# Optimization experiments

Hardware: AMD Instinct MI355X
Metric: run time of the kernel (lower is better)

The kernel has to match this reference:

```python
import jax, jax.numpy as jnp
import numpy as np
from jax import lax

NEG_INF = -1e18
T, K, U = 8192, 24, 104


def setup_inputs() -> dict:
    key = jax.random.key(0)
    k1, k2, k3, k4, k5 = jax.random.split(key, 5)
    emission_logprobs = jax.random.normal(k1, (T, K), dtype=jnp.float32)
    quality_weights = jax.random.uniform(k2, (T,), dtype=jnp.float32)
    log_pi = jax.nn.log_softmax(jax.random.normal(k3, (K,), dtype=jnp.float32))
    log_A = jax.nn.log_softmax(jax.random.normal(k4, (K, K), dtype=jnp.float32), axis=1)
    log_D = jax.nn.log_softmax(jax.random.normal(k5, (K, U), dtype=jnp.float32), axis=1)
    # explicit-duration HSMM: self-transitions disallowed (durations model dwell time)
    transition_mask = 1 - jnp.eye(K, dtype=jnp.int32)
    return {"emission_logprobs": emission_logprobs, "quality_weights": quality_weights,
            "log_pi": log_pi, "log_A": log_A, "log_D": log_D,
            "transition_mask": transition_mask}


def _segment_scores(emission, qw):
    # seg[t, u_idx, s] = sum_{k=t-u+1..t} qw[k]*B[k,s], u = u_idx+1; NEG_INF if u > t+1
    weighted = emission * qw[:, None]
    cum = jnp.concatenate([jnp.zeros((1, K), emission.dtype), jnp.cumsum(weighted, 0)], 0)  # [T+1,K]
    t_idx = jnp.arange(T)
    u = jnp.arange(1, U + 1)
    start = t_idx[:, None] + 1 - u[None, :]              # [T,U]
    valid = start >= 0
    seg = cum[t_idx + 1][:, None, :] - cum[jnp.clip(start, 0)]  # [T,U,K]
    return jnp.where(valid[:, :, None], seg, NEG_INF)


def _forward_backward(emission, qw, log_pi, log_A_m, log_D):
    seg = _segment_scores(emission, qw)  # [T,U,K]
    log_D_T = log_D.T                    # [U,K]
    u_idx = jnp.arange(U)

    # ---- forward DP over t (carry = last U alpha rows) ----
    alpha0 = log_pi + log_D[:, 0] + emission[0]
    buf0 = jnp.full((U, K), NEG_INF, emission.dtype).at[-1].set(alpha0)

    def fstep(buf, t):
        prev = buf[::-1]  # prev[u_idx] = alpha[t-1-u_idx] (NEG_INF for times < 0)
        trans = jax.nn.logsumexp(prev[:, :, None] + log_A_m[None, :, :], axis=1)  # [U,K]
        # entry_time = t-1-u_idx < 0  <=>  u_idx >= t : use initial-state score
        inner = jnp.where((u_idx >= t)[:, None], log_pi[None, :], trans)
        alpha_t = jax.nn.logsumexp(inner + log_D_T + seg[t], axis=0)  # [K]
        return jnp.concatenate([buf[1:], alpha_t[None]], 0), alpha_t

    _, alphas = lax.scan(fstep, buf0, jnp.arange(1, T))
    alpha = jnp.concatenate([alpha0[None], alphas], 0)

    # ---- backward DP (carry buf[i] = beta[t+1+i]) ----
    bbuf0 = jnp.full((U, K), NEG_INF, emission.dtype).at[0].set(0.0)

    def bstep(buf, t):
        ends = t + 1 + u_idx
        valid = ends <= T - 1
        segv = seg[jnp.clip(ends, 0, T - 1), u_idx, :]                 # [U,K]
        inner = jnp.where(valid[:, None], log_D_T + segv + buf, NEG_INF)
        m = jax.nn.logsumexp(inner, axis=0)                            # [K] over durations
        beta_t = jax.nn.logsumexp(log_A_m + m[None, :], axis=1)        # [K] over next state
        return jnp.concatenate([beta_t[None], buf[:-1]], 0), beta_t

    _, betas = lax.scan(bstep, bbuf0, jnp.arange(T - 2, -1, -1))
    beta = jnp.concatenate([betas[::-1], jnp.zeros((1, K), emission.dtype)], 0)
    return alpha, beta


def reference(emission_logprobs, quality_weights, log_pi, log_A, log_D, transition_mask):
    log_A_m = jnp.where(transition_mask.astype(bool), log_A, NEG_INF)
    alpha, beta = _forward_backward(emission_logprobs, quality_weights, log_pi, log_A_m, log_D)
    # posterior_decode: gamma = alpha + beta, normalized over states
    return jax.nn.softmax(alpha + beta, axis=1)
```

## Files before the change

### kernel.cpp

```cpp
#include <hip/hip_runtime.h>
#include <math.h>

#define TT 8192
#define KK 24
#define UU 104
#define NEGINF (-1e18f)
#define INV_LN2 1.4426950408889634f

__device__ __forceinline__ float exp2_(float x) {
#if __has_builtin(__builtin_amdgcn_exp2f)
  return __builtin_amdgcn_exp2f(x);
#else
  return exp2f(x);
#endif
}

template<int CTRL>
__device__ __forceinline__ float dppf(float x) {
  return __builtin_bit_cast(float,
    __builtin_amdgcn_update_dpp(0, __builtin_bit_cast(int, x), CTRL, 0xF, 0xF, true));
}
__device__ __forceinline__ float red16_sum(float v) {
  v += dppf<0xB1>(v);
  v += dppf<0x4E>(v);
  v += dppf<0x124>(v);
  v += dppf<0x128>(v);
  return v;
}
__device__ __forceinline__ float ror1(float x) { return dppf<0x121>(x); }

__global__ __launch_bounds__(256) void cumsum_kernel(
    const float* __restrict__ em, const float* __restrict__ qw,
    float* __restrict__ cum)
{
  const int k = blockIdx.x;
  const int tid = threadIdx.x;
  const int lane = tid & 63;
  const int wid = tid >> 6;
  __shared__ float wsum[4];
  float carry = 0.0f;
  if (tid == 0) cum[k] = 0.0f;
  for (int c = 0; c < TT / 256; ++c) {
    int t = c * 256 + tid;
    float v = em[t * KK + k] * (qw[t] * INV_LN2);
    #pragma unroll
    for (int d = 1; d < 64; d <<= 1) {
      float tmp = __shfl_up(v, d);
      if (lane >= d) v += tmp;
    }
    if (lane == 63) wsum[wid] = v;
    __syncthreads();
    float off = carry;
    #pragma unroll
    for (int w = 0; w < 4; ++w)
      if (w < wid) off += wsum[w];
    cum[(size_t)(t + 1) * KK + k] = off + v;
    carry += wsum[0] + wsum[1] + wsum[2] + wsum[3];
    __syncthreads();
  }
}

__global__ __launch_bounds__(384, 1) void scan_kernel(
    const float* __restrict__ em,
    const float* __restrict__ log_pi,
    const float* __restrict__ log_A,
    const float* __restrict__ log_D,
    const float* __restrict__ cum,
    float* __restrict__ alpha_out,
    float* __restrict__ beta_out)
{
  __shared__ __align__(16) float xbuf[2][32];
  const int tid = threadIdx.x;
  const int g = tid >> 4;
  const int L = tid & 15;
  const bool l0 = (L == 0);
  const int j1 = 2 * L, j2 = 2 * L + 1;

  if (tid < 8) { xbuf[0][24 + tid] = 0.0f; xbuf[1][24 + tid] = 0.0f; }

  float ld0 = log_D[g * UU + L] * INV_LN2;
  float ld1 = log_D[g * UU + L + 16] * INV_LN2;
  float ld2 = log_D[g * UU + L + 32] * INV_LN2;
  float ld3 = log_D[g * UU + L + 48] * INV_LN2;
  float ld4 = log_D[g * UU + L + 64] * INV_LN2;
  float ld5 = log_D[g * UU + L + 80] * INV_LN2;
  float ld6 = (L < 8) ? log_D[g * UU + L + 96] * INV_LN2 : NEGINF;

  if (blockIdx.x == 0) {
    float Ak1 = (j1 < KK && j1 != g) ? log_A[j1 * KK + g] * INV_LN2 : NEGINF;
    float Ak2 = (j2 < KK && j2 != g) ? log_A[j2 * KK + g] * INV_LN2 : NEGINF;
    float lpi2 = log_pi[g] * INV_LN2;
    float a0 = lpi2 + log_D[g * UU] * INV_LN2 + em[g] * INV_LN2;
    if (l0) { alpha_out[g] = a0; xbuf[0][g] = a0; }
    float P0 = l0 ? lpi2 : NEGINF;
    float P1 = NEGINF, P2 = NEGINF, P3 = NEGINF,
          P4 = NEGINF, P5 = NEGINF, P6 = NEGINF;
    float ccur = cum[1 * KK + g], c1 = cum[2 * KK + g],
          c2 = cum[3 * KK + g],  c3 = cum[4 * KK + g];
    float Mh = a0;
    float Ua = a0 - ccur;
    __syncthreads();
    for (int t = 1; t < TT; ++t) {
      int tp = t + 4; if (tp > TT) tp = TT;
      float c4 = cum[(size_t)tp * KK + g];
      float r0 = ror1(P0), r1 = ror1(P1), r2 = ror1(P2), r3 = ror1(P3),
            r4 = ror1(P4), r5 = ror1(P5), r6 = ror1(P6);
      P1 = l0 ? r0 : r1;  P2 = l0 ? r1 : r2;  P3 = l0 ? r2 : r3;
      P4 = l0 ? r3 : r4;  P5 = l0 ? r4 : r5;  P6 = l0 ? r5 : r6;
      float e1 = exp2_(P1 + (ld1 - Ua));
      float e2 = exp2_(P2 + (ld2 - Ua));
      float e3 = exp2_(P3 + (ld3 - Ua));
      float e4 = exp2_(P4 + (ld4 - Ua));
      float e5 = exp2_(P5 + (ld5 - Ua));
      float e6 = exp2_(P6 + (ld6 - Ua));
      float e0nz = exp2_(r0 + (ld0 - Ua));
      float srest = ((e1 + e2) + (e3 + e4)) + (e5 + e6);
      float2 av = *(const float2*)&xbuf[(t - 1) & 1][j1];
      float w1 = av.x + (Ak1 - Mh);
      float w2 = av.y + (Ak2 - Mh);
      float s1 = red16_sum(exp2_(w1) + exp2_(w2));
      float gamma = Mh + __log2f(s1);
      Mh = gamma;
      float phi = gamma - ccur;
      P0 = l0 ? phi : r0;
      float e0 = l0 ? exp2_(phi + (ld0 - Ua)) : e0nz;
      float S = red16_sum(e0 + srest);
      float ua = Ua + __log2f(S);
      float a = c1 + ua;
      Ua = ua;
      if (l0) { xbuf[t & 1][g] = a; alpha_out[(size_t)t * KK + g] = a; }
      ccur = c1; c1 = c2; c2 = c3; c3 = c4;
      __syncthreads();
    }
  } else {
    float Bj1 = (j1 < KK && j1 != g) ? log_A[g * KK + j1] * INV_LN2 : NEGINF;
    float Bj2 = (j2 < KK && j2 != g) ? log_A[g * KK + j2] * INV_LN2 : NEGINF;
    float cT = cum[(size_t)TT * KK + g];
    if (l0) beta_out[(size_t)(TT - 1) * KK + g] = 0.0f;
    float Q0 = l0 ? cT : NEGINF;
    float Q1 = NEGINF, Q2 = NEGINF, Q3 = NEGINF,
          Q4 = NEGINF, Q5 = NEGINF, Q6 = NEGINF;
    float c1 = cum[(size_t)(TT - 1) * KK + g];
    float d1 = cum[(size_t)(TT - 2) * KK + g];
    float d2 = cum[(size_t)(TT - 3) * KK + g];
    float nh = cT;
    float bh = 0.0f;
    __syncthreads();
    for (int t = TT - 2; t >= 0; --t) {
      int tp = t - 2; if (tp < 0) tp = 0;
      float d3 = cum[(size_t)tp * KK + g];
      float x0 = exp2_(Q0 + (ld0 - nh));
      float x1 = exp2_(Q1 + (ld1 - nh));
      float x2 = exp2_(Q2 + (ld2 - nh));
      float x3 = exp2_(Q3 + (ld3 - nh));
      float x4 = exp2_(Q4 + (ld4 - nh));
      float x5 = exp2_(Q5 + (ld5 - nh));
      float x6 = exp2_(Q6 + (ld6 - nh));
      float sA = red16_sum(((x0 + x1) + (x2 + x3)) + ((x4 + x5) + x6));
      float n = nh + __log2f(sA);
      nh = n;
      float m = n - c1;
      if (l0) xbuf[t & 1][g] = m;
      __syncthreads();
      float2 mv = *(const float2*)&xbuf[t & 1][j1];
      float y1 = mv.x + (Bj1 - bh);
      float y2 = mv.y + (Bj2 - bh);
      float sB = red16_sum(exp2_(y1) + exp2_(y2));
      float bt = bh + __log2f(sB);
      bh = bt;
      float psi = c1 + bt;
      if (l0) beta_out[(size_t)t * KK + g] = bt;
      float q0 = ror1(Q0), q1 = ror1(Q1), q2 = ror1(Q2), q3 = ror1(Q3),
            q4 = ror1(Q4), q5 = ror1(Q5), q6 = ror1(Q6);
      Q6 = l0 ? q5 : q6;  Q5 = l0 ? q4 : q5;  Q4 = l0 ? q3 : q4;
      Q3 = l0 ? q2 : q3;  Q2 = l0 ? q1 : q2;  Q1 = l0 ? q0 : q1;
      Q0 = l0 ? psi : q0;
      c1 = d1; d1 = d2; d2 = d3;
    }
  }
}

__global__ __launch_bounds__(256) void softmax_kernel(
    float* __restrict__ ab, const float* __restrict__ beta)
{
  int t = blockIdx.x * 256 + threadIdx.x;
  float s[KK];
  float mx = -INFINITY;
  #pragma unroll
  for (int k = 0; k < KK; ++k) {
    s[k] = ab[(size_t)t * KK + k] + beta[(size_t)t * KK + k];
    mx = fmaxf(mx, s[k]);
  }
  float sum = 0.0f;
  #pragma unroll
  for (int k = 0; k < KK; ++k) { s[k] = exp2_(s[k] - mx); sum += s[k]; }
  float inv = 1.0f / sum;
  #pragma unroll
  for (int k = 0; k < KK; ++k) ab[(size_t)t * KK + k] = s[k] * inv;
}

extern "C" void kernel_launch(void* const* d_in, const int* in_sizes, int n_in,
                              void* d_out, int out_size, void* d_ws, size_t ws_size,
                              hipStream_t stream) {
  const float* em  = (const float*)d_in[0];
  const float* qw  = (const float*)d_in[1];
  const float* lpi = (const float*)d_in[2];
  const float* lA  = (const float*)d_in[3];
  const float* lD  = (const float*)d_in[4];

  float* out  = (float*)d_out;
  float* cum  = (float*)d_ws;
  float* beta = (float*)d_ws + (size_t)(TT + 1) * KK;

  cumsum_kernel<<<KK, 256, 0, stream>>>(em, qw, cum);
  scan_kernel<<<2, 384, 0, stream>>>(em, lpi, lA, lD, cum, out, beta);
  softmax_kernel<<<TT / 256, 256, 0, stream>>>(out, beta);
}
```

Before: 3.740 ms.

## Restructure HSMM scans to exchange linear-domain sums and shorten serial chain

Both forward and backward recurrences are reformulated so that the value exchanged through shared memory each step is a linear-domain normalized sum rather than a log value. Each lane tracks the per-state running log offsets of its neighbour states itself, so the exp/log work that used to sit between barriers is moved off the critical path. The per-step dependent chain becomes FMA plus DPP reduction plus a shared store and barrier, with the exps for the next step computed after the barrier. In exchange it adds clamping (CLMP, 1e-37 floors) and extra log2 calls per step, which carries some numerical risk under large dynamic range.

Result: slower. 4.765 ms (+27.4%).

```diff
diff --git a/kernel.cpp b/kernel.cpp
--- a/kernel.cpp
+++ b/kernel.cpp
@@ -6,6 +6,7 @@
 #define UU 104
 #define NEGINF (-1e18f)
 #define INV_LN2 1.4426950408889634f
+#define CLMP 60.0f
 
 __device__ __forceinline__ float exp2_(float x) {
 #if __has_builtin(__builtin_amdgcn_exp2f)
@@ -28,6 +29,14 @@
   return v;
 }
 __device__ __forceinline__ float ror1(float x) { return dppf<0x121>(x); }
+
+__device__ __forceinline__ float a0_of(const float* lp, const float* lD,
+                                       const float* em, int s) {
+  return (lp[s] * INV_LN2 + lD[s * UU] * INV_LN2) + em[s] * INV_LN2;
+}
+__device__ __forceinline__ float nh0_of(const float* lD, const float* cum, int s) {
+  return lD[s * UU] * INV_LN2 + cum[(size_t)TT * KK + s];
+}
 
 __global__ __launch_bounds__(256) void cumsum_kernel(
     const float* __restrict__ em, const float* __restrict__ qw,
@@ -75,8 +84,10 @@
   const int L = tid & 15;
   const bool l0 = (L == 0);
   const int j1 = 2 * L, j2 = 2 * L + 1;
-
-  if (tid < 8) { xbuf[0][24 + tid] = 0.0f; xbuf[1][24 + tid] = 0.0f; }
+  const bool vj = (j1 < KK);
+  const int jc = vj ? j1 : 0;
+
+  if (tid < 8) { xbuf[0][24 + tid] = 1.0f; xbuf[1][24 + tid] = 1.0f; }
 
   float ld0 = log_D[g * UU + L] * INV_LN2;
   float ld1 = log_D[g * UU + L + 16] * INV_LN2;
@@ -85,97 +96,169 @@
   float ld4 = log_D[g * UU + L + 64] * INV_LN2;
   float ld5 = log_D[g * UU + L + 80] * INV_LN2;
   float ld6 = (L < 8) ? log_D[g * UU + L + 96] * INV_LN2 : NEGINF;
+  float d0 = log_D[g * UU] * INV_LN2;
 
   if (blockIdx.x == 0) {
-    float Ak1 = (j1 < KK && j1 != g) ? log_A[j1 * KK + g] * INV_LN2 : NEGINF;
-    float Ak2 = (j2 < KK && j2 != g) ? log_A[j2 * KK + g] * INV_LN2 : NEGINF;
+    float Ak1 = (vj && j1 != g) ? log_A[j1 * KK + g] * INV_LN2 : NEGINF;
+    float Ak2 = (vj && j2 != g) ? log_A[j2 * KK + g] * INV_LN2 : NEGINF;
     float lpi2 = log_pi[g] * INV_LN2;
-    float a0 = lpi2 + log_D[g * UU] * INV_LN2 + em[g] * INV_LN2;
-    if (l0) { alpha_out[g] = a0; xbuf[0][g] = a0; }
+    float a0 = a0_of(log_pi, log_D, em, g);
+    float cc0 = cum[1 * KK + g], cc1 = cum[2 * KK + g],
+          cc2 = cum[3 * KK + g], cc3 = cum[4 * KK + g];
+    float2 pj1r = *(const float2*)&cum[1 * KK + jc];
+    float2 pjA = *(const float2*)&cum[2 * KK + jc];
+    float2 pjB = *(const float2*)&cum[3 * KK + jc];
+    float2 pjC = *(const float2*)&cum[4 * KK + jc];
+    float Ua = a0 - cc0;
+    float Uaj1 = vj ? (a0_of(log_pi, log_D, em, j1) - pj1r.x) : 0.f;
+    float Uaj2 = vj ? (a0_of(log_pi, log_D, em, j2) - pj1r.y) : 0.f;
+    float Mh = a0;
+    float f1 = exp2_(fminf((pj1r.x + Uaj1) + (Ak1 - Mh), CLMP));
+    float f2 = exp2_(fminf((pj1r.y + Uaj2) + (Ak2 - Mh), CLMP));
+    float fc = exp2_(fminf((Mh + d0) - (cc0 + Ua), CLMP));
+    float fc0 = l0 ? fc : 0.f;
     float P0 = l0 ? lpi2 : NEGINF;
     float P1 = NEGINF, P2 = NEGINF, P3 = NEGINF,
           P4 = NEGINF, P5 = NEGINF, P6 = NEGINF;
-    float ccur = cum[1 * KK + g], c1 = cum[2 * KK + g],
-          c2 = cum[3 * KK + g],  c3 = cum[4 * KK + g];
-    float Mh = a0;
-    float Ua = a0 - ccur;
-    __syncthreads();
-    for (int t = 1; t < TT; ++t) {
-      int tp = t + 4; if (tp > TT) tp = TT;
-      float c4 = cum[(size_t)tp * KK + g];
+    {
       float r0 = ror1(P0), r1 = ror1(P1), r2 = ror1(P2), r3 = ror1(P3),
             r4 = ror1(P4), r5 = ror1(P5), r6 = ror1(P6);
+      P0 = r0;
       P1 = l0 ? r0 : r1;  P2 = l0 ? r1 : r2;  P3 = l0 ? r2 : r3;
       P4 = l0 ? r3 : r4;  P5 = l0 ? r4 : r5;  P6 = l0 ? r5 : r6;
-      float e1 = exp2_(P1 + (ld1 - Ua));
-      float e2 = exp2_(P2 + (ld2 - Ua));
-      float e3 = exp2_(P3 + (ld3 - Ua));
-      float e4 = exp2_(P4 + (ld4 - Ua));
-      float e5 = exp2_(P5 + (ld5 - Ua));
-      float e6 = exp2_(P6 + (ld6 - Ua));
-      float e0nz = exp2_(r0 + (ld0 - Ua));
-      float srest = ((e1 + e2) + (e3 + e4)) + (e5 + e6);
-      float2 av = *(const float2*)&xbuf[(t - 1) & 1][j1];
-      float w1 = av.x + (Ak1 - Mh);
-      float w2 = av.y + (Ak2 - Mh);
-      float s1 = red16_sum(exp2_(w1) + exp2_(w2));
-      float gamma = Mh + __log2f(s1);
-      Mh = gamma;
-      float phi = gamma - ccur;
-      P0 = l0 ? phi : r0;
-      float e0 = l0 ? exp2_(phi + (ld0 - Ua)) : e0nz;
-      float S = red16_sum(e0 + srest);
-      float ua = Ua + __log2f(S);
-      float a = c1 + ua;
-      Ua = ua;
-      if (l0) { xbuf[t & 1][g] = a; alpha_out[(size_t)t * KK + g] = a; }
-      ccur = c1; c1 = c2; c2 = c3; c3 = c4;
+    }
+    float mU = 0.f - Ua;
+    float e0 = exp2_(P0 + (ld0 + mU));
+    float e1 = exp2_(P1 + (ld1 + mU));
+    float e2 = exp2_(P2 + (ld2 + mU));
+    float e3 = exp2_(P3 + (ld3 + mU));
+    float e4 = exp2_(P4 + (ld4 + mU));
+    float e5 = exp2_(P5 + (ld5 + mU));
+    float e6 = exp2_(P6 + (ld6 + mU));
+    float sloc = (((l0 ? 0.f : e0) + e1) + (e2 + e3)) + ((e4 + e5) + e6);
+    if (l0) alpha_out[g] = a0;
+    float2 Sjr; Sjr.x = 1.0f; Sjr.y = 1.0f;
+    __syncthreads();
+    #pragma unroll 1
+    for (int t = 1; t < TT; ++t) {
+      float w  = fmaf(Sjr.x, f1, Sjr.y * f2);
+      float sG = red16_sum(w);
+      float vv = fmaf(sG, fc0, sloc);
+      float S  = red16_sum(vv);
+      float Sp = fmaxf(S, 1e-37f);
+      if (l0) xbuf[t & 1][g] = Sp;
       __syncthreads();
+      float2 Sjn = *(const float2*)&xbuf[t & 1][j1];
+      int tp = (t + 4 <= TT) ? (t + 4) : TT;
+      float ccN = cum[(size_t)tp * KK + g];
+      float2 pjN = *(const float2*)&cum[(size_t)tp * KK + jc];
+      float lgG = __log2f(fmaxf(sG, 1e-37f));
+      float lgS = __log2f(Sp);
+      Mh += lgG;
+      float phi = Mh - cc0;
+      if (l0) alpha_out[(size_t)t * KK + g] = (cc1 + Ua) + lgS;
+      Ua += lgS;
+      Uaj1 += __log2f(Sjr.x);
+      Uaj2 += __log2f(Sjr.y);
+      f1 = exp2_(fminf((pjA.x + Uaj1) + (Ak1 - Mh), CLMP));
+      f2 = exp2_(fminf((pjA.y + Uaj2) + (Ak2 - Mh), CLMP));
+      fc = exp2_(fminf((Mh + d0) - (cc1 + Ua), CLMP));
+      fc0 = l0 ? fc : 0.f;
+      float P0i = l0 ? phi : P0;
+      float r0 = ror1(P0i), r1 = ror1(P1), r2 = ror1(P2), r3 = ror1(P3),
+            r4 = ror1(P4), r5 = ror1(P5), r6 = ror1(P6);
+      P0 = r0;
+      P1 = l0 ? r0 : r1;  P2 = l0 ? r1 : r2;  P3 = l0 ? r2 : r3;
+      P4 = l0 ? r3 : r4;  P5 = l0 ? r4 : r5;  P6 = l0 ? r5 : r6;
+      float mU2 = 0.f - Ua;
+      e0 = exp2_(P0 + (ld0 + mU2));
+      e1 = exp2_(P1 + (ld1 + mU2));
+      e2 = exp2_(P2 + (ld2 + mU2));
+      e3 = exp2_(P3 + (ld3 + mU2));
+      e4 = exp2_(P4 + (ld4 + mU2));
+      e5 = exp2_(P5 + (ld5 + mU2));
+      e6 = exp2_(P6 + (ld6 + mU2));
+      sloc = (((l0 ? 0.f : e0) + e1) + (e2 + e3)) + ((e4 + e5) + e6);
+      Sjr = Sjn;
+      cc0 = cc1; cc1 = cc2; cc2 = cc3; cc3 = ccN;
+      pjA = pjB; pjB = pjC; pjC = pjN;
     }
   } else {
-    float Bj1 = (j1 < KK && j1 != g) ? log_A[g * KK + j1] * INV_LN2 : NEGINF;
-    float Bj2 = (j2 < KK && j2 != g) ? log_A[g * KK + j2] * INV_LN2 : NEGINF;
+    float Cj1 = (vj && j1 != g) ? log_A[g * KK + j1] * INV_LN2 : NEGINF;
+    float Cj2 = (vj && j2 != g) ? log_A[g * KK + j2] * INV_LN2 : NEGINF;
     float cT = cum[(size_t)TT * KK + g];
-    if (l0) beta_out[(size_t)(TT - 1) * KK + g] = 0.0f;
+    float cA = cum[(size_t)(TT - 1) * KK + g];
+    float cB = cum[(size_t)(TT - 2) * KK + g];
+    float cC = cum[(size_t)(TT - 3) * KK + g];
+    float2 pj1b = *(const float2*)&cum[(size_t)(TT - 1) * KK + jc];
+    float2 pjB = *(const float2*)&cum[(size_t)(TT - 2) * KK + jc];
+    float2 pjC = *(const float2*)&cum[(size_t)(TT - 3) * KK + jc];
+    float Nh = nh0_of(log_D, cum, g);
+    float Nhj1 = vj ? nh0_of(log_D, cum, j1) : 0.f;
+    float Nhj2 = vj ? nh0_of(log_D, cum, j2) : 0.f;
+    float bh = 0.0f;
+    float f1 = exp2_(fminf((Nhj1 - pj1b.x) + Cj1, CLMP));
+    float f2 = exp2_(fminf((Nhj2 - pj1b.y) + Cj2, CLMP));
     float Q0 = l0 ? cT : NEGINF;
     float Q1 = NEGINF, Q2 = NEGINF, Q3 = NEGINF,
           Q4 = NEGINF, Q5 = NEGINF, Q6 = NEGINF;
-    float c1 = cum[(size_t)(TT - 1) * KK + g];
-    float d1 = cum[(size_t)(TT - 2) * KK + g];
-    float d2 = cum[(size_t)(TT - 3) * KK + g];
-    float nh = cT;
-    float bh = 0.0f;
+    float mN = 0.f - Nh;
+    float e0 = exp2_(Q0 + (ld0 + mN));
+    float e1 = exp2_(Q1 + (ld1 + mN));
+    float e2 = exp2_(Q2 + (ld2 + mN));
+    float e3 = exp2_(Q3 + (ld3 + mN));
+    float e4 = exp2_(Q4 + (ld4 + mN));
+    float e5 = exp2_(Q5 + (ld5 + mN));
+    float e6 = exp2_(Q6 + (ld6 + mN));
+    float slocB = ((e0 + e1) + (e2 + e3)) + ((e4 + e5) + e6);
+    float fb = 0.f, fb0 = 0.f, sBprev = 0.f;
+    float psi_prev = cT;
+    if (l0) beta_out[(size_t)(TT - 1) * KK + g] = 0.0f;
     __syncthreads();
+    #pragma unroll 1
     for (int t = TT - 2; t >= 0; --t) {
-      int tp = t - 2; if (tp < 0) tp = 0;
-      float d3 = cum[(size_t)tp * KK + g];
-      float x0 = exp2_(Q0 + (ld0 - nh));
-      float x1 = exp2_(Q1 + (ld1 - nh));
-      float x2 = exp2_(Q2 + (ld2 - nh));
-      float x3 = exp2_(Q3 + (ld3 - nh));
-      float x4 = exp2_(Q4 + (ld4 - nh));
-      float x5 = exp2_(Q5 + (ld5 - nh));
-      float x6 = exp2_(Q6 + (ld6 - nh));
-      float sA = red16_sum(((x0 + x1) + (x2 + x3)) + ((x4 + x5) + x6));
-      float n = nh + __log2f(sA);
-      nh = n;
-      float m = n - c1;
-      if (l0) xbuf[t & 1][g] = m;
+      float vA = fmaf(sBprev, fb0, slocB);
+      float SA = red16_sum(vA);
+      float SAp = fmaxf(SA, 1e-37f);
+      if (l0) xbuf[t & 1][g] = SAp;
       __syncthreads();
-      float2 mv = *(const float2*)&xbuf[t & 1][j1];
-      float y1 = mv.x + (Bj1 - bh);
-      float y2 = mv.y + (Bj2 - bh);
-      float sB = red16_sum(exp2_(y1) + exp2_(y2));
-      float bt = bh + __log2f(sB);
+      float2 SAj = *(const float2*)&xbuf[t & 1][j1];
+      int tm = (t - 2 >= 0) ? (t - 2) : 0;
+      float cN = cum[(size_t)tm * KK + g];
+      float2 pjN = *(const float2*)&cum[(size_t)tm * KK + jc];
+      float wb = fmaf(SAj.x, f1, SAj.y * f2);
+      float sB = red16_sum(wb);
+      float lgA = __log2f(SAp);
+      float lgB = __log2f(fmaxf(sB, 1e-37f));
+      Nh += lgA;
+      float bt = bh + lgB;
+      if (l0) beta_out[(size_t)t * KK + g] = bt;
+      fb = exp2_(fminf(((d0 + cA) + bh) - Nh, CLMP));
+      fb0 = l0 ? fb : 0.f;
       bh = bt;
-      float psi = c1 + bt;
-      if (l0) beta_out[(size_t)t * KK + g] = bt;
-      float q0 = ror1(Q0), q1 = ror1(Q1), q2 = ror1(Q2), q3 = ror1(Q3),
-            q4 = ror1(Q4), q5 = ror1(Q5), q6 = ror1(Q6);
-      Q6 = l0 ? q5 : q6;  Q5 = l0 ? q4 : q5;  Q4 = l0 ? q3 : q4;
-      Q3 = l0 ? q2 : q3;  Q2 = l0 ? q1 : q2;  Q1 = l0 ? q0 : q1;
-      Q0 = l0 ? psi : q0;
-      c1 = d1; d1 = d2; d2 = d3;
+      Nhj1 += __log2f(SAj.x);
+      Nhj2 += __log2f(SAj.y);
+      f1 = exp2_(fminf((Nhj1 - pjB.x) + (Cj1 - bh), CLMP));
+      f2 = exp2_(fminf((Nhj2 - pjB.y) + (Cj2 - bh), CLMP));
+      float Q0i = l0 ? psi_prev : Q0;
+      float r0 = ror1(Q0i), r1 = ror1(Q1), r2 = ror1(Q2), r3 = ror1(Q3),
+            r4 = ror1(Q4), r5 = ror1(Q5), r6 = ror1(Q6);
+      Q0 = r0;
+      Q1 = l0 ? r0 : r1;  Q2 = l0 ? r1 : r2;  Q3 = l0 ? r2 : r3;
+      Q4 = l0 ? r3 : r4;  Q5 = l0 ? r4 : r5;  Q6 = l0 ? r5 : r6;
+      psi_prev = cA + bt;
+      float mN2 = 0.f - Nh;
+      e0 = exp2_(Q0 + (ld0 + mN2));
+      e1 = exp2_(Q1 + (ld1 + mN2));
+      e2 = exp2_(Q2 + (ld2 + mN2));
+      e3 = exp2_(Q3 + (ld3 + mN2));
+      e4 = exp2_(Q4 + (ld4 + mN2));
+      e5 = exp2_(Q5 + (ld5 + mN2));
+      e6 = exp2_(Q6 + (ld6 + mN2));
+      slocB = (((l0 ? 0.f : e0) + e1) + (e2 + e3)) + ((e4 + e5) + e6);
+      sBprev = sB;
+      cA = cB; cB = cC; cC = cN;
+      pjB = pjC; pjC = pjN;
     }
   }
 }
```

## Halve scan lanes per state and shorten serial critical path per timestep

Applied to the files above, without the earlier changes.

Each state now uses 8 lanes instead of 16, so the scan block shrinks from 384 to 192 threads and each lane holds 13 duration slots, with a custom ror9 DPP used to shift the history ring. The forward step is reordered so the duration-sum over older entries is precomputed off the critical path and combined with the transition sum in one fused multiply-add. This leaves a single reduction and log per step before the barrier. The backward step likewise precomputes its duration sum, and a lighter barrier that only waits on LDS replaces __syncthreads. The exp2 argument is clamped at 60 and sums are floored before the log, which risks small numerical differences and adds more exp2 work per lane.

Result: faster. 3.562 ms (-4.8%).

```diff
diff --git a/kernel.cpp b/kernel.cpp
--- a/kernel.cpp
+++ b/kernel.cpp
@@ -6,6 +6,7 @@
 #define UU 104
 #define NEGINF (-1e18f)
 #define INV_LN2 1.4426950408889634f
+#define CLMP 60.0f
 
 __device__ __forceinline__ float exp2_(float x) {
 #if __has_builtin(__builtin_amdgcn_exp2f)
@@ -15,19 +16,25 @@
 #endif
 }
 
+__device__ __forceinline__ void wg_barrier() {
+  asm volatile("s_waitcnt lgkmcnt(0)" ::: "memory");
+  __builtin_amdgcn_s_barrier();
+  asm volatile("" ::: "memory");
+}
+
 template<int CTRL>
 __device__ __forceinline__ float dppf(float x) {
   return __builtin_bit_cast(float,
     __builtin_amdgcn_update_dpp(0, __builtin_bit_cast(int, x), CTRL, 0xF, 0xF, true));
 }
-__device__ __forceinline__ float red16_sum(float v) {
+__device__ __forceinline__ float red8_sum(float v) {
   v += dppf<0xB1>(v);
   v += dppf<0x4E>(v);
-  v += dppf<0x124>(v);
-  v += dppf<0x128>(v);
+  v += dppf<0x141>(v);
   return v;
 }
 __device__ __forceinline__ float ror1(float x) { return dppf<0x121>(x); }
+__device__ __forceinline__ float ror9(float x) { return dppf<0x129>(x); }
 
 __global__ __launch_bounds__(256) void cumsum_kernel(
     const float* __restrict__ em, const float* __restrict__ qw,
@@ -60,7 +67,7 @@
   }
 }
 
-__global__ __launch_bounds__(384, 1) void scan_kernel(
+__global__ __launch_bounds__(192, 1) void scan_kernel(
     const float* __restrict__ em,
     const float* __restrict__ log_pi,
     const float* __restrict__ log_A,
@@ -69,113 +76,213 @@
     float* __restrict__ alpha_out,
     float* __restrict__ beta_out)
 {
-  __shared__ __align__(16) float xbuf[2][32];
+  __shared__ __align__(16) float xb[2][32];
   const int tid = threadIdx.x;
-  const int g = tid >> 4;
-  const int L = tid & 15;
+  const int g = tid >> 3;
+  const int L = tid & 7;
   const bool l0 = (L == 0);
-  const int j1 = 2 * L, j2 = 2 * L + 1;
-
-  if (tid < 8) { xbuf[0][24 + tid] = 0.0f; xbuf[1][24 + tid] = 0.0f; }
-
-  float ld0 = log_D[g * UU + L] * INV_LN2;
-  float ld1 = log_D[g * UU + L + 16] * INV_LN2;
-  float ld2 = log_D[g * UU + L + 32] * INV_LN2;
-  float ld3 = log_D[g * UU + L + 48] * INV_LN2;
-  float ld4 = log_D[g * UU + L + 64] * INV_LN2;
-  float ld5 = log_D[g * UU + L + 80] * INV_LN2;
-  float ld6 = (L < 8) ? log_D[g * UU + L + 96] * INV_LN2 : NEGINF;
+
+  if (tid < 8) { xb[0][24 + tid] = 0.0f; xb[1][24 + tid] = 0.0f; }
+
+  const int jb = 4 * L;
+  float Ak0, Ak1, Ak2, Ak3;
+  float d0 = log_D[g * UU] * INV_LN2;
 
   if (blockIdx.x == 0) {
-    float Ak1 = (j1 < KK && j1 != g) ? log_A[j1 * KK + g] * INV_LN2 : NEGINF;
-    float Ak2 = (j2 < KK && j2 != g) ? log_A[j2 * KK + g] * INV_LN2 : NEGINF;
+    float LD[13];
+    #pragma unroll
+    for (int i = 0; i < 13; ++i) {
+      int u = L + 8 * i + 1;
+      LD[i] = (u <= 103) ? log_D[g * UU + u] * INV_LN2 : NEGINF;
+    }
+    Ak0 = (jb + 0 < KK && jb + 0 != g) ? log_A[(jb + 0) * KK + g] * INV_LN2 : NEGINF;
+    Ak1 = (jb + 1 < KK && jb + 1 != g) ? log_A[(jb + 1) * KK + g] * INV_LN2 : NEGINF;
+    Ak2 = (jb + 2 < KK && jb + 2 != g) ? log_A[(jb + 2) * KK + g] * INV_LN2 : NEGINF;
+    Ak3 = (jb + 3 < KK && jb + 3 != g) ? log_A[(jb + 3) * KK + g] * INV_LN2 : NEGINF;
+
     float lpi2 = log_pi[g] * INV_LN2;
-    float a0 = lpi2 + log_D[g * UU] * INV_LN2 + em[g] * INV_LN2;
-    if (l0) { alpha_out[g] = a0; xbuf[0][g] = a0; }
-    float P0 = l0 ? lpi2 : NEGINF;
-    float P1 = NEGINF, P2 = NEGINF, P3 = NEGINF,
-          P4 = NEGINF, P5 = NEGINF, P6 = NEGINF;
-    float ccur = cum[1 * KK + g], c1 = cum[2 * KK + g],
-          c2 = cum[3 * KK + g],  c3 = cum[4 * KK + g];
+    float a0 = (lpi2 + d0) + em[g] * INV_LN2;
+    if (l0) { xb[0][g] = a0; alpha_out[g] = a0; }
     float Mh = a0;
-    float Ua = a0 - ccur;
+    float cc0 = cum[1 * KK + g], cc1 = cum[2 * KK + g],
+          cc2 = cum[3 * KK + g], cc3 = cum[4 * KK + g];
+    float Ua = a0 - cc0;
+    float P0 = (tid % 8 == 0 && true) ? 0.0f : 0.0f;
+    float P1, P2, P3, P4, P5, P6, P7, P8, P9, P10, P11, P12;
+    P0 = l0 ? lpi2 : NEGINF;
+    P1 = P2 = P3 = P4 = P5 = P6 = P7 = P8 = P9 = P10 = P11 = P12 = NEGINF;
+    float mUa = 0.f - Ua;
+    float sloc;
+    {
+      float e0  = exp2_(P0  + (LD[0]  + mUa));
+      float e1  = exp2_(P1  + (LD[1]  + mUa));
+      float e2  = exp2_(P2  + (LD[2]  + mUa));
+      float e3  = exp2_(P3  + (LD[3]  + mUa));
+      float e4  = exp2_(P4  + (LD[4]  + mUa));
+      float e5  = exp2_(P5  + (LD[5]  + mUa));
+      float e6  = exp2_(P6  + (LD[6]  + mUa));
+      float e7  = exp2_(P7  + (LD[7]  + mUa));
+      float e8  = exp2_(P8  + (LD[8]  + mUa));
+      float e9  = exp2_(P9  + (LD[9]  + mUa));
+      float e10 = exp2_(P10 + (LD[10] + mUa));
+      float e11 = exp2_(P11 + (LD[11] + mUa));
+      float e12 = exp2_(P12 + (LD[12] + mUa));
+      sloc = (((e0 + e1) + (e2 + e3)) + ((e4 + e5) + (e6 + e7))) +
+             (((e8 + e9) + (e10 + e11)) + e12);
+    }
+    float Akm0 = Ak0 - Mh, Akm1 = Ak1 - Mh, Akm2 = Ak2 - Mh, Akm3 = Ak3 - Mh;
+    float fc0 = l0 ? exp2_(fminf((Mh + d0) - (cc0 + Ua), CLMP)) : 0.0f;
     __syncthreads();
+    #pragma unroll 1
     for (int t = 1; t < TT; ++t) {
-      int tp = t + 4; if (tp > TT) tp = TT;
-      float c4 = cum[(size_t)tp * KK + g];
-      float r0 = ror1(P0), r1 = ror1(P1), r2 = ror1(P2), r3 = ror1(P3),
-            r4 = ror1(P4), r5 = ror1(P5), r6 = ror1(P6);
-      P1 = l0 ? r0 : r1;  P2 = l0 ? r1 : r2;  P3 = l0 ? r2 : r3;
-      P4 = l0 ? r3 : r4;  P5 = l0 ? r4 : r5;  P6 = l0 ? r5 : r6;
-      float e1 = exp2_(P1 + (ld1 - Ua));
-      float e2 = exp2_(P2 + (ld2 - Ua));
-      float e3 = exp2_(P3 + (ld3 - Ua));
-      float e4 = exp2_(P4 + (ld4 - Ua));
-      float e5 = exp2_(P5 + (ld5 - Ua));
-      float e6 = exp2_(P6 + (ld6 - Ua));
-      float e0nz = exp2_(r0 + (ld0 - Ua));
-      float srest = ((e1 + e2) + (e3 + e4)) + (e5 + e6);
-      float2 av = *(const float2*)&xbuf[(t - 1) & 1][j1];
-      float w1 = av.x + (Ak1 - Mh);
-      float w2 = av.y + (Ak2 - Mh);
-      float s1 = red16_sum(exp2_(w1) + exp2_(w2));
-      float gamma = Mh + __log2f(s1);
+      float4 S4 = *(const float4*)&xb[(t - 1) & 1][jb];
+      int tp = (t + 4 <= TT) ? (t + 4) : TT;
+      float ccN = cum[(size_t)tp * KK + g];
+      float w0 = S4.x + Akm0, w1 = S4.y + Akm1,
+            w2 = S4.z + Akm2, w3 = S4.w + Akm3;
+      float sG = red8_sum((exp2_(w0) + exp2_(w1)) + (exp2_(w2) + exp2_(w3)));
+      float vv = fmaf(sG, fc0, sloc);
+      float S  = red8_sum(vv);
+      float Sp = fmaxf(S, 1e-37f);
+      float lgS = __log2f(Sp);
+      float a = (cc1 + Ua) + lgS;
+      if (l0) xb[t & 1][g] = a;
+      wg_barrier();
+      if (l0) alpha_out[(size_t)t * KK + g] = a;
+      float lgG = __log2f(fmaxf(sG, 1e-37f));
+      float gamma = Mh + lgG;
       Mh = gamma;
-      float phi = gamma - ccur;
-      P0 = l0 ? phi : r0;
-      float e0 = l0 ? exp2_(phi + (ld0 - Ua)) : e0nz;
-      float S = red16_sum(e0 + srest);
-      float ua = Ua + __log2f(S);
-      float a = c1 + ua;
-      Ua = ua;
-      if (l0) { xbuf[t & 1][g] = a; alpha_out[(size_t)t * KK + g] = a; }
-      ccur = c1; c1 = c2; c2 = c3; c3 = c4;
-      __syncthreads();
+      float phi = gamma - cc0;
+      Ua += lgS;
+      Akm0 = Ak0 - Mh; Akm1 = Ak1 - Mh; Akm2 = Ak2 - Mh; Akm3 = Ak3 - Mh;
+      fc0 = l0 ? exp2_(fminf((Mh + d0) - (cc1 + Ua), CLMP)) : 0.0f;
+      float r0 = ror1(P0),  r1 = ror1(P1),  r2 = ror1(P2),  r3 = ror1(P3),
+            r4 = ror1(P4),  r5 = ror1(P5),  r6 = ror1(P6),  r7 = ror1(P7),
+            r8 = ror1(P8),  r9 = ror1(P9),  r10 = ror1(P10), r11 = ror1(P11),
+            r12 = ror1(P12);
+      float q1 = ror9(P0),  q2 = ror9(P1),  q3 = ror9(P2),  q4 = ror9(P3),
+            q5 = ror9(P4),  q6 = ror9(P5),  q7 = ror9(P6),  q8 = ror9(P7),
+            q9 = ror9(P8),  q10 = ror9(P9), q11 = ror9(P10), q12 = ror9(P11);
+      P0  = l0 ? phi : r0;
+      P1  = l0 ? q1  : r1;   P2  = l0 ? q2  : r2;
+      P3  = l0 ? q3  : r3;   P4  = l0 ? q4  : r4;
+      P5  = l0 ? q5  : r5;   P6  = l0 ? q6  : r6;
+      P7  = l0 ? q7  : r7;   P8  = l0 ? q8  : r8;
+      P9  = l0 ? q9  : r9;   P10 = l0 ? q10 : r10;
+      P11 = l0 ? q11 : r11;  P12 = l0 ? q12 : r12;
+      float mU = 0.f - Ua;
+      float e0  = exp2_(P0  + (LD[0]  + mU));
+      float e1  = exp2_(P1  + (LD[1]  + mU));
+      float e2  = exp2_(P2  + (LD[2]  + mU));
+      float e3  = exp2_(P3  + (LD[3]  + mU));
+      float e4  = exp2_(P4  + (LD[4]  + mU));
+      float e5  = exp2_(P5  + (LD[5]  + mU));
+      float e6  = exp2_(P6  + (LD[6]  + mU));
+      float e7  = exp2_(P7  + (LD[7]  + mU));
+      float e8  = exp2_(P8  + (LD[8]  + mU));
+      float e9  = exp2_(P9  + (LD[9]  + mU));
+      float e10 = exp2_(P10 + (LD[10] + mU));
+      float e11 = exp2_(P11 + (LD[11] + mU));
+      float e12 = exp2_(P12 + (LD[12] + mU));
+      sloc = (((e0 + e1) + (e2 + e3)) + ((e4 + e5) + (e6 + e7))) +
+             (((e8 + e9) + (e10 + e11)) + e12);
+      cc0 = cc1; cc1 = cc2; cc2 = cc3; cc3 = ccN;
     }
   } else {
-    float Bj1 = (j1 < KK && j1 != g) ? log_A[g * KK + j1] * INV_LN2 : NEGINF;
-    float Bj2 = (j2 < KK && j2 != g) ? log_A[g * KK + j2] * INV_LN2 : NEGINF;
+    float LD[13];
+    #pragma unroll
+    for (int i = 0; i < 13; ++i)
+      LD[i] = log_D[g * UU + (L + 8 * i)] * INV_LN2;
+    Ak0 = (jb + 0 < KK && jb + 0 != g) ? log_A[g * KK + (jb + 0)] * INV_LN2 : NEGINF;
+    Ak1 = (jb + 1 < KK && jb + 1 != g) ? log_A[g * KK + (jb + 1)] * INV_LN2 : NEGINF;
+    Ak2 = (jb + 2 < KK && jb + 2 != g) ? log_A[g * KK + (jb + 2)] * INV_LN2 : NEGINF;
+    Ak3 = (jb + 3 < KK && jb + 3 != g) ? log_A[g * KK + (jb + 3)] * INV_LN2 : NEGINF;
+
     float cT = cum[(size_t)TT * KK + g];
     if (l0) beta_out[(size_t)(TT - 1) * KK + g] = 0.0f;
+    float Nh = cT + d0;
+    float bh = 0.0f;
+    float cA = cum[(size_t)(TT - 1) * KK + g];
+    float cB = cum[(size_t)(TT - 2) * KK + g];
+    float cC = cum[(size_t)(TT - 3) * KK + g];
     float Q0 = l0 ? cT : NEGINF;
-    float Q1 = NEGINF, Q2 = NEGINF, Q3 = NEGINF,
-          Q4 = NEGINF, Q5 = NEGINF, Q6 = NEGINF;
-    float c1 = cum[(size_t)(TT - 1) * KK + g];
-    float d1 = cum[(size_t)(TT - 2) * KK + g];
-    float d2 = cum[(size_t)(TT - 3) * KK + g];
-    float nh = cT;
-    float bh = 0.0f;
+    float Q1 = NEGINF, Q2 = NEGINF, Q3 = NEGINF, Q4 = NEGINF, Q5 = NEGINF,
+          Q6 = NEGINF, Q7 = NEGINF, Q8 = NEGINF, Q9 = NEGINF, Q10 = NEGINF,
+          Q11 = NEGINF, Q12 = NEGINF;
+    float slocB;
+    {
+      float mN = 0.f - Nh;
+      float e0  = exp2_(Q0  + (LD[0]  + mN));
+      float e1  = exp2_(Q1  + (LD[1]  + mN));
+      float e2  = exp2_(Q2  + (LD[2]  + mN));
+      float e3  = exp2_(Q3  + (LD[3]  + mN));
+      float e4  = exp2_(Q4  + (LD[4]  + mN));
+      float e5  = exp2_(Q5  + (LD[5]  + mN));
+      float e6  = exp2_(Q6  + (LD[6]  + mN));
+      float e7  = exp2_(Q7  + (LD[7]  + mN));
+      float e8  = exp2_(Q8  + (LD[8]  + mN));
+      float e9  = exp2_(Q9  + (LD[9]  + mN));
+      float e10 = exp2_(Q10 + (LD[10] + mN));
+      float e11 = exp2_(Q11 + (LD[11] + mN));
+      float e12 = exp2_(Q12 + (LD[12] + mN));
+      slocB = (((e0 + e1) + (e2 + e3)) + ((e4 + e5) + (e6 + e7))) +
+              (((e8 + e9) + (e10 + e11)) + e12);
+    }
+    float Cm0 = Ak0 - bh, Cm1 = Ak1 - bh, Cm2 = Ak2 - bh, Cm3 = Ak3 - bh;
     __syncthreads();
+    #pragma unroll 1
     for (int t = TT - 2; t >= 0; --t) {
-      int tp = t - 2; if (tp < 0) tp = 0;
-      float d3 = cum[(size_t)tp * KK + g];
-      float x0 = exp2_(Q0 + (ld0 - nh));
-      float x1 = exp2_(Q1 + (ld1 - nh));
-      float x2 = exp2_(Q2 + (ld2 - nh));
-      float x3 = exp2_(Q3 + (ld3 - nh));
-      float x4 = exp2_(Q4 + (ld4 - nh));
-      float x5 = exp2_(Q5 + (ld5 - nh));
-      float x6 = exp2_(Q6 + (ld6 - nh));
-      float sA = red16_sum(((x0 + x1) + (x2 + x3)) + ((x4 + x5) + x6));
-      float n = nh + __log2f(sA);
-      nh = n;
-      float m = n - c1;
-      if (l0) xbuf[t & 1][g] = m;
-      __syncthreads();
-      float2 mv = *(const float2*)&xbuf[t & 1][j1];
-      float y1 = mv.x + (Bj1 - bh);
-      float y2 = mv.y + (Bj2 - bh);
-      float sB = red16_sum(exp2_(y1) + exp2_(y2));
-      float bt = bh + __log2f(sB);
+      float SA = red8_sum(slocB);
+      float SAp = fmaxf(SA, 1e-37f);
+      float lgA = __log2f(SAp);
+      float n = Nh + lgA;
+      float m = n - cA;
+      if (l0) xb[t & 1][g] = m;
+      wg_barrier();
+      float4 m4 = *(const float4*)&xb[t & 1][jb];
+      int tm = (t - 2 >= 0) ? (t - 2) : 0;
+      float cN = cum[(size_t)tm * KK + g];
+      float y0 = m4.x + Cm0, y1 = m4.y + Cm1,
+            y2 = m4.z + Cm2, y3 = m4.w + Cm3;
+      float sB = red8_sum((exp2_(y0) + exp2_(y1)) + (exp2_(y2) + exp2_(y3)));
+      float lgB = __log2f(fmaxf(sB, 1e-37f));
+      float bt = bh + lgB;
+      if (l0) beta_out[(size_t)t * KK + g] = bt;
+      Nh = n;
+      float psi = cA + bt;
       bh = bt;
-      float psi = c1 + bt;
-      if (l0) beta_out[(size_t)t * KK + g] = bt;
-      float q0 = ror1(Q0), q1 = ror1(Q1), q2 = ror1(Q2), q3 = ror1(Q3),
-            q4 = ror1(Q4), q5 = ror1(Q5), q6 = ror1(Q6);
-      Q6 = l0 ? q5 : q6;  Q5 = l0 ? q4 : q5;  Q4 = l0 ? q3 : q4;
-      Q3 = l0 ? q2 : q3;  Q2 = l0 ? q1 : q2;  Q1 = l0 ? q0 : q1;
-      Q0 = l0 ? psi : q0;
-      c1 = d1; d1 = d2; d2 = d3;
+      Cm0 = Ak0 - bh; Cm1 = Ak1 - bh; Cm2 = Ak2 - bh; Cm3 = Ak3 - bh;
+      float r0 = ror1(Q0),  r1 = ror1(Q1),  r2 = ror1(Q2),  r3 = ror1(Q3),
+            r4 = ror1(Q4),  r5 = ror1(Q5),  r6 = ror1(Q6),  r7 = ror1(Q7),
+            r8 = ror1(Q8),  r9 = ror1(Q9),  r10 = ror1(Q10), r11 = ror1(Q11),
+            r12 = ror1(Q12);
+      float q1 = ror9(Q0),  q2 = ror9(Q1),  q3 = ror9(Q2),  q4 = ror9(Q3),
+            q5 = ror9(Q4),  q6 = ror9(Q5),  q7 = ror9(Q6),  q8 = ror9(Q7),
+            q9 = ror9(Q8),  q10 = ror9(Q9), q11 = ror9(Q10), q12 = ror9(Q11);
+      Q0  = l0 ? psi : r0;
+      Q1  = l0 ? q1  : r1;   Q2  = l0 ? q2  : r2;
+      Q3  = l0 ? q3  : r3;   Q4  = l0 ? q4  : r4;
+      Q5  = l0 ? q5  : r5;   Q6  = l0 ? q6  : r6;
+      Q7  = l0 ? q7  : r7;   Q8  = l0 ? q8  : r8;
+      Q9  = l0 ? q9  : r9;   Q10 = l0 ? q10 : r10;
+      Q11 = l0 ? q11 : r11;  Q12 = l0 ? q12 : r12;
+      float mN = 0.f - Nh;
+      float e0  = exp2_(Q0  + (LD[0]  + mN));
+      float e1  = exp2_(Q1  + (LD[1]  + mN));
+      float e2  = exp2_(Q2  + (LD[2]  + mN));
+      float e3  = exp2_(Q3  + (LD[3]  + mN));
+      float e4  = exp2_(Q4  + (LD[4]  + mN));
+      float e5  = exp2_(Q5  + (LD[5]  + mN));
+      float e6  = exp2_(Q6  + (LD[6]  + mN));
+      float e7  = exp2_(Q7  + (LD[7]  + mN));
+      float e8  = exp2_(Q8  + (LD[8]  + mN));
+      float e9  = exp2_(Q9  + (LD[9]  + mN));
+      float e10 = exp2_(Q10 + (LD[10] + mN));
+      float e11 = exp2_(Q11 + (LD[11] + mN));
+      float e12 = exp2_(Q12 + (LD[12] + mN));
+      slocB = (((e0 + e1) + (e2 + e3)) + ((e4 + e5) + (e6 + e7))) +
+              (((e8 + e9) + (e10 + e11)) + e12);
+      cA = cB; cB = cC; cC = cN;
     }
   }
 }
@@ -213,6 +320,6 @@
   float* beta = (float*)d_ws + (size_t)(TT + 1) * KK;
 
   cumsum_kernel<<<KK, 256, 0, stream>>>(em, qw, cum);
-  scan_kernel<<<2, 384, 0, stream>>>(em, lpi, lA, lD, cum, out, beta);
+  scan_kernel<<<2, 192, 0, stream>>>(em, lpi, lA, lD, cum, out, beta);
   softmax_kernel<<<TT / 256, 256, 0, stream>>>(out, beta);
 }
```
